# Kernel tuning notes

Hardware: AMD Instinct MI355X
Metric: run time of the kernel (lower is better)

The kernel has to match this reference:

```python
import jax, jax.numpy as jnp
import numpy as np

B, C, H, W = 8, 3, 64, 64

def _abs2relu(x):
    return 2.0 * jax.nn.relu(x) - x

def _tent(offset):
    # matches RotationPerturbationLayer._tent_weights: relu(1 - |offset|)
    z = 1.0 - _abs2relu(offset)
    return 0.5 * (z + _abs2relu(z))

def setup_inputs() -> dict:
    key = jax.random.key(0)
    k1, k2 = jax.random.split(key)
    theta = jax.random.normal(k1, (B, 1), dtype=jnp.float32)  # rotation angles
    image = jax.random.normal(k2, (C, H, W), dtype=jnp.float32)
    return {"theta": theta, "image": image}

def reference(theta, image):
    Cc, Hh, Ww = image.shape
    N = Hh * Ww
    c_x = (Ww - 1) / 2.0
    c_y = (Hh - 1) / 2.0
    xs = jnp.arange(Ww, dtype=jnp.float32)
    ys = jnp.arange(Hh, dtype=jnp.float32)
    grid_y, grid_x = jnp.meshgrid(ys, xs, indexing='ij')
    x_rel = (grid_x - c_x).reshape(1, -1)  # [1, N]
    y_rel = (grid_y - c_y).reshape(1, -1)  # [1, N]

    cos_t = jnp.cos(theta)  # [B, 1]
    sin_t = jnp.sin(theta)
    src_x = cos_t * x_rel + sin_t * y_rel + c_x   # [B, N]
    src_y = -sin_t * x_rel + cos_t * y_rel + c_y  # [B, N]

    wx = _tent(src_x[..., None] - xs)  # [B, N, W]
    wy = _tent(src_y[..., None] - ys)  # [B, N, H]
    # outer product over (H, W) then flatten -> dense tent-weight mask per coord
    wxy = wy[:, :, :, None] * wx[:, :, None, :]          # [B, N, H, W]
    w_flat = wxy.reshape(theta.shape[0], N, N)           # [B, N, num_pixels]
    flat_img = image.reshape(Cc, N)                      # [C, num_pixels]
    sampled = jnp.einsum('bnp,cp->bcn', w_flat, flat_img)  # Linear(num_pixels->C)
    return sampled.reshape(theta.shape[0], Cc, Hh, Ww)
```

## Files before the change

kernel.cpp:

```cpp
#include <hip/hip_runtime.h>
#include <math.h>

#define BB 8
#define CC 3
#define HH 64
#define WW 64
#define NN (HH * WW)

__global__ __launch_bounds__(256) void rot_bilinear_kernel(
        const float* __restrict__ theta,
        const float* __restrict__ image,
        float* __restrict__ out) {
    int tid = blockIdx.x * blockDim.x + threadIdx.x;
    if (tid >= BB * NN) return;

    int b  = tid >> 12;
    int n  = tid & (NN - 1);
    int gy = n >> 6;
    int gx = n & (WW - 1);

    const float c_x = (WW - 1) * 0.5f;
    const float c_y = (HH - 1) * 0.5f;

    float t = theta[b];
    float s, c;
    __sincosf(t, &s, &c);

    float x_rel = (float)gx - c_x;
    float y_rel = (float)gy - c_y;
    float src_x = fmaf(c, x_rel, fmaf(s, y_rel, c_x));
    float src_y = fmaf(-s, x_rel, fmaf(c, y_rel, c_y));

    float fx = floorf(src_x);
    float fy = floorf(src_y);
    int x0 = (int)fx;
    int y0 = (int)fy;
    float ax = src_x - fx;
    float ay = src_y - fy;
    float bx = 1.0f - ax;
    float by = 1.0f - ay;

    bool vx0 = (unsigned)x0       < (unsigned)WW;
    bool vx1 = (unsigned)(x0 + 1) < (unsigned)WW;
    bool vy0 = (unsigned)y0       < (unsigned)HH;
    bool vy1 = (unsigned)(y0 + 1) < (unsigned)HH;
    float wx0 = vx0 ? bx : 0.0f;
    float wx1 = vx1 ? ax : 0.0f;
    float wy0 = vy0 ? by : 0.0f;
    float wy1 = vy1 ? ay : 0.0f;
    float w00 = wy0 * wx0;
    float w01 = wy0 * wx1;
    float w10 = wy1 * wx0;
    float w11 = wy1 * wx1;

    int x0c = min(max(x0, 0), WW - 1);
    int x1c = min(max(x0 + 1, 0), WW - 1);
    int y0c = min(max(y0, 0), HH - 1);
    int y1c = min(max(y0 + 1, 0), HH - 1);
    int i00 = y0c * WW + x0c;
    int i01 = y0c * WW + x1c;
    int i10 = y1c * WW + x0c;
    int i11 = y1c * WW + x1c;

    const float* img = image;
    float* o = out + b * CC * NN + n;
    #pragma unroll
    for (int ch = 0; ch < CC; ++ch, img += NN, o += NN) {
        float v = w00 * img[i00] + w01 * img[i01]
                + w10 * img[i10] + w11 * img[i11];
        *o = v;
    }
}

extern "C" void kernel_launch(void* const* d_in, const int* in_sizes, int n_in,
                              void* d_out, int out_size, void* d_ws, size_t ws_size,
                              hipStream_t stream) {
    const float* theta = (const float*)d_in[0];
    const float* image = (const float*)d_in[1];
    float* out = (float*)d_out;

    const int total = BB * NN;
    const int block = 256;
    const int grid  = (total + block - 1) / block;
    rot_bilinear_kernel<<<grid, block, 0, stream>>>(theta, image, out);
}
```

Measured before the change: 55.34 us.

## Stage full image in swizzled LDS via async global-to-LDS loads

Each block asynchronously copies the entire 3-channel image into shared memory using global_load_lds with an XOR swizzle to reduce bank conflicts, then performs bilinear gathers from LDS. Block size drops to 128 and the grid is fixed at 256. This removes scattered global gathers but makes every block load the whole image, adding redundant L2 traffic and a sync before any compute.

```diff
diff --git a/kernel.cpp b/kernel.cpp
--- a/kernel.cpp
+++ b/kernel.cpp
@@ -6,25 +6,43 @@
 #define HH 64
 #define WW 64
 #define NN (HH * WW)
+#define IMG_FLOATS (CC * NN)
 
-__global__ __launch_bounds__(256) void rot_bilinear_kernel(
+__global__ __launch_bounds__(128) void rot_bilinear_kernel(
         const float* __restrict__ theta,
         const float* __restrict__ image,
         float* __restrict__ out) {
-    int tid = blockIdx.x * blockDim.x + threadIdx.x;
-    if (tid >= BB * NN) return;
+    __shared__ float simg[IMG_FLOATS];
 
-    int b  = tid >> 12;
-    int n  = tid & (NN - 1);
-    int gy = n >> 6;
-    int gx = n & (WW - 1);
+    const int t    = threadIdx.x;
+    const int wv   = t >> 6;
+    const int lane = t & 63;
+
+    #pragma unroll
+    for (int it = 0; it < 24; ++it) {
+        int d     = it * 512 + wv * 256 + lane * 4;
+        int chunk = d >> 2;
+        int r     = chunk >> 4;
+        int slot  = chunk & 15;
+        int sfl   = ((r << 4) | (slot ^ (r & 15))) << 2;
+        __builtin_amdgcn_global_load_lds(
+            (const __attribute__((address_space(1))) void*)(image + sfl),
+            (__attribute__((address_space(3))) void*)(simg + it * 512 + wv * 256),
+            16, 0, 0);
+    }
+
+    const int bid = blockIdx.x;
+    const int b   = bid >> 5;
+    const int n   = ((bid & 31) << 7) + t;
+    const int gy  = n >> 6;
+    const int gx  = n & (WW - 1);
 
     const float c_x = (WW - 1) * 0.5f;
     const float c_y = (HH - 1) * 0.5f;
 
-    float t = theta[b];
+    float th = theta[b];
     float s, c;
-    __sincosf(t, &s, &c);
+    __sincosf(th, &s, &c);
 
     float x_rel = (float)gx - c_x;
     float y_rel = (float)gy - c_y;
@@ -57,17 +75,22 @@
     int x1c = min(max(x0 + 1, 0), WW - 1);
     int y0c = min(max(y0, 0), HH - 1);
     int y1c = min(max(y0 + 1, 0), HH - 1);
-    int i00 = y0c * WW + x0c;
-    int i01 = y0c * WW + x1c;
-    int i10 = y1c * WW + x0c;
-    int i11 = y1c * WW + x1c;
 
-    const float* img = image;
-    float* o = out + b * CC * NN + n;
+    int m0 = y0c & 15, m1 = y1c & 15;
+    int s0 = x0c >> 2, s1 = x1c >> 2;
+    int i00 = (y0c << 6) | ((s0 ^ m0) << 2) | (x0c & 3);
+    int i01 = (y0c << 6) | ((s1 ^ m0) << 2) | (x1c & 3);
+    int i10 = (y1c << 6) | ((s0 ^ m1) << 2) | (x0c & 3);
+    int i11 = (y1c << 6) | ((s1 ^ m1) << 2) | (x1c & 3);
+
+    __syncthreads();
+
+    const float* sc = simg;
+    float* o = out + b * (CC * NN) + n;
     #pragma unroll
-    for (int ch = 0; ch < CC; ++ch, img += NN, o += NN) {
-        float v = w00 * img[i00] + w01 * img[i01]
-                + w10 * img[i10] + w11 * img[i11];
+    for (int ch = 0; ch < CC; ++ch, sc += NN, o += NN) {
+        float v = w00 * sc[i00] + w01 * sc[i01]
+                + w10 * sc[i10] + w11 * sc[i11];
         *o = v;
     }
 }
@@ -79,8 +102,7 @@
     const float* image = (const float*)d_in[1];
     float* out = (float*)d_out;
 
-    const int total = BB * NN;
-    const int block = 256;
-    const int grid  = (total + block - 1) / block;
+    const int block = 128;
+    const int grid  = 256;
     rot_bilinear_kernel<<<grid, block, 0, stream>>>(theta, image, out);
 }
```

New measurement: 55.63 us. About the same (+0.5%).
